# Performance work log

Measured on AMD Instinct MI355X. Metric: run time of the kernel, lower is better.

The kernel has to match this reference:

```python
import jax, jax.numpy as jnp
import numpy as np

DIM, HEADS, B, HT, WD = 96, 8, 4, 160, 160


def conv2d(x, w, b=None, padding=0, groups=1):
    out = jax.lax.conv_general_dilated(
        x, w, (1, 1), [(padding, padding), (padding, padding)],
        dimension_numbers=('NCHW', 'OIHW', 'NCHW'), feature_group_count=groups)
    if b is not None:
        out = out + b[None, :, None, None]
    return out


def setup_inputs() -> dict:
    key = jax.random.key(0)
    ks = jax.random.split(key, 16)
    dim, H = DIM, HEADS
    p = lambda i, shape: jax.random.normal(ks[i], shape, jnp.float32) * 0.05
    return {
        'x': jax.random.normal(ks[0], (B, dim, HT, WD), jnp.float32),
        'spectral': jax.random.normal(ks[1], (B, dim), jnp.float32),
        'temperature': jnp.ones((H, 1, 1), jnp.float32),
        'w_qkv': p(2, (3 * dim, dim, 1, 1)),           # 1x1x1 conv3d == 1x1 conv2d (depth=1)
        'w_dw': p(3, (3 * dim, 1, 3, 3)),              # middle depth slice of 3x3x3 dwconv
        'w_proj': p(4, (dim, dim, 1, 1)),
        'w_fc': p(5, (9, 3 * H)), 'b_fc': jnp.zeros((9,), jnp.float32),
        'w_dep': p(6, (dim, 9, 3, 3)), 'b_dep': jnp.zeros((dim,), jnp.float32),
        'w_se1': p(7, (2 * dim, dim)), 'b_se1': jnp.zeros((2 * dim,), jnp.float32),
        'w_se2': p(8, (dim, 2 * dim)), 'b_se2': jnp.zeros((dim,), jnp.float32),
        'w_saw1': p(9, (dim // 4, 1, 3, 3)), 'b_saw1': jnp.zeros((dim // 4,), jnp.float32),
        'w_saw2': p(10, (HEADS, dim // 4, 1, 1)), 'b_saw2': jnp.zeros((HEADS,), jnp.float32),
        'w_sgp': p(11, (dim, dim)), 'b_sgp': jnp.zeros((dim,), jnp.float32),
    }


def reference(x, spectral, temperature, w_qkv, w_dw, w_proj, w_fc, b_fc,
              w_dep, b_dep, w_se1, b_se1, w_se2, b_se2,
              w_saw1, b_saw1, w_saw2, b_saw2, w_sgp, b_sgp):
    b, c, h, w = x.shape
    H = temperature.shape[0]
    cH = c // H
    # spectral enhance gate: Linear -> GELU -> Linear -> Sigmoid
    sw = jax.nn.sigmoid(
        jax.nn.gelu(spectral @ w_se1.T + b_se1, approximate=False) @ w_se2.T + b_se2)
    x = x * sw[:, :, None, None]
    # qkv: 1x1 conv then 3x3 depthwise (depth-1 3D conv collapses to 2D middle slice)
    qkv = conv2d(conv2d(x, w_qkv), w_dw, padding=1, groups=3 * c)  # (b,3c,h,w)
    # fc branch: reshape (b,3c,h,w) -> (b,hw,3H,cH) -> (b,3H,hw,cH); 1x1 conv over 3H
    f_all = qkv.reshape(b, h * w, 3 * H, cH).transpose(0, 2, 1, 3)
    f_all = jnp.einsum('oc,bcnd->bond', w_fc, f_all) + b_fc[None, :, None, None]  # (b,9,hw,cH)
    f_conv = f_all.transpose(0, 3, 1, 2).reshape(b, 9 * cH, h, w)
    out_conv = conv2d(f_conv, w_dep, b_dep, padding=1, groups=cH)  # (b,c,h,w)
    # channel attention path
    q, k, v = jnp.split(qkv, 3, axis=1)
    resh = lambda t: t.reshape(b, H, cH, h * w)
    q, k, v = resh(q), resh(k), resh(v)
    sg = (spectral @ w_sgp.T + b_sgp).reshape(b, H, cH)
    cm = x.mean(axis=(1, 2, 3), keepdims=True)                      # (b,1,1,1)
    cm_exp = jnp.broadcast_to(cm, (b, 1, h, w))
    saw = jax.nn.sigmoid(conv2d(
        jax.nn.gelu(conv2d(cm_exp, w_saw1, b_saw1, padding=1), approximate=False),
        w_saw2, b_saw2))                                            # (b,H,h,w)
    saw = saw.mean(axis=(2, 3))[..., None]                          # (b,H,1)
    esg = sg * saw                                                  # (b,H,cH)
    sgm = esg[..., :, None] * esg[..., None, :]                     # (b,H,cH,cH)
    qn = q / jnp.maximum(jnp.linalg.norm(q, axis=-1, keepdims=True), 1e-12)
    kn = k / jnp.maximum(jnp.linalg.norm(k, axis=-1, keepdims=True), 1e-12)
    attn = jnp.einsum('bhcn,bhdn->bhcd', qn, kn) * temperature[None]
    attn = jax.nn.softmax(attn * sgm, axis=-1)
    out = jnp.einsum('bhcd,bhdn->bhcn', attn, v).reshape(b, c, h, w)
    out = conv2d(out, w_proj)
    return out + out_conv
```

## Files before the change

### kernel.cpp

```cpp
#include <hip/hip_runtime.h>
#include <math.h>

#define NB 4
#define C 96
#define C3 288
#define NH 8
#define CHD 12
#define HT 160
#define WD 160
#define HW 25600

typedef unsigned short u16;
typedef unsigned int   u32;
typedef __bf16 bf16x8 __attribute__((ext_vector_type(8)));
typedef float  f32x4  __attribute__((ext_vector_type(4)));

__device__ __forceinline__ float gelu_f(float x){
    return 0.5f * x * (1.0f + erff(x * 0.7071067811865475f));
}
__device__ __forceinline__ float sigmoid_f(float x){
    return 1.0f / (1.0f + expf(-x));
}
__device__ __forceinline__ u16 f2bf(float x){
    union { float f; u32 u; } v; v.f = x;
    u32 r = v.u + 0x7FFFu + ((v.u >> 16) & 1u);
    return (u16)(r >> 16);
}
__device__ __forceinline__ float bf2f(u16 s){
    union { u32 u; float f; } v; v.u = ((u32)s) << 16;
    return v.f;
}

__global__ __launch_bounds__(256) void k0_xsum(const float* __restrict__ x,
                                               float* __restrict__ xsum,
                                               u16* __restrict__ xb){
    int bc = blockIdx.x;
    const float4* p4 = (const float4*)(x + (size_t)bc * HW);
    u32* xo = (u32*)(xb + (size_t)bc * HW);
    float s = 0.f;
    for (int i = threadIdx.x; i < HW/4; i += 256){
        float4 v = p4[i];
        s += (v.x + v.y) + (v.z + v.w);
        xo[i*2]   = (u32)f2bf(v.x) | ((u32)f2bf(v.y) << 16);
        xo[i*2+1] = (u32)f2bf(v.z) | ((u32)f2bf(v.w) << 16);
    }
    __shared__ float red[256];
    red[threadIdx.x] = s;
    __syncthreads();
    for (int off = 128; off > 0; off >>= 1){
        if (threadIdx.x < off) red[threadIdx.x] += red[threadIdx.x + off];
        __syncthreads();
    }
    if (threadIdx.x == 0) xsum[bc] = red[0];
}

__global__ void k1_small(const float* __restrict__ spectral, const float* __restrict__ xsum,
                         const float* __restrict__ w_se1, const float* __restrict__ b_se1,
                         const float* __restrict__ w_se2, const float* __restrict__ b_se2,
                         const float* __restrict__ w_saw1, const float* __restrict__ b_saw1,
                         const float* __restrict__ w_saw2, const float* __restrict__ b_saw2,
                         const float* __restrict__ w_sgp, const float* __restrict__ b_sgp,
                         float* __restrict__ swg, float* __restrict__ esgg){
    __shared__ float spec[96];
    __shared__ float h1[192];
    __shared__ float cm_s;
    __shared__ float g1[9][24];
    __shared__ float saw[8];
    __shared__ float redbuf[96];
    int t = threadIdx.x;
    int b = blockIdx.x;
    if (t < 96) spec[t] = spectral[b*96 + t];
    __syncthreads();
    if (t < 192){
        float a = b_se1[t];
        for (int c = 0; c < 96; c++) a += spec[c] * w_se1[t*96 + c];
        h1[t] = gelu_f(a);
    }
    __syncthreads();
    if (t < 96){
        float a = b_se2[t];
        for (int j = 0; j < 192; j++) a += h1[j] * w_se2[t*192 + j];
        float s = sigmoid_f(a);
        swg[b*96 + t] = s;
        redbuf[t] = s * xsum[b*96 + t];
    }
    __syncthreads();
    if (t == 0){
        float cs = 0.f;
        for (int c = 0; c < 96; c++) cs += redbuf[c];
        cm_s = cs / (96.0f * (float)HW);
    }
    __syncthreads();
    float cm = cm_s;
    if (t < 9*24){
        int cat = t / 24, ch = t % 24;
        int ti = cat / 3, tj = cat % 3;
        float S = 0.f;
        for (int ki = 0; ki < 3; ki++){
            if (ti == 0 && ki == 0) continue;
            if (ti == 2 && ki == 2) continue;
            for (int kj = 0; kj < 3; kj++){
                if (tj == 0 && kj == 0) continue;
                if (tj == 2 && kj == 2) continue;
                S += w_saw1[ch*9 + ki*3 + kj];
            }
        }
        g1[cat][ch] = gelu_f(cm * S + b_saw1[ch]);
    }
    __syncthreads();
    if (t < 8){
        float acc = 0.f;
        const float cnt[3] = {1.f, 158.f, 1.f};
        for (int cat = 0; cat < 9; cat++){
            float a = b_saw2[t];
            for (int ch = 0; ch < 24; ch++) a += w_saw2[t*24 + ch] * g1[cat][ch];
            acc += cnt[cat/3] * cnt[cat%3] * sigmoid_f(a);
        }
        saw[t] = acc / (float)HW;
    }
    __syncthreads();
    if (t < 96){
        float a = b_sgp[t];
        for (int j = 0; j < 96; j++) a += spec[j] * w_sgp[t*96 + j];
        esgg[b*96 + t] = a * saw[t/12];
    }
}

__global__ __launch_bounds__(256) void k1w_weff(const float* __restrict__ w_qkv,
                                                const float* __restrict__ swg,
                                                u16* __restrict__ weffb){
    int b = blockIdx.x;
    int i = blockIdx.y * 256 + threadIdx.x;
    float w = w_qkv[i] * swg[b*96 + (i % 96)];
    weffb[(size_t)b*C3*96 + i] = f2bf(w);
}

__global__ __launch_bounds__(384) void k2a_mfma(const u16* __restrict__ xb,
                                                const u16* __restrict__ weffb,
                                                u16* __restrict__ Y,
                                                int bbase, long ystride){
    int b   = bbase + blockIdx.y;
    int px0 = blockIdx.x * 64;
    __shared__ u16 Xl[64*128];
    int t = threadIdx.x;
    const u32* xsrc = (const u32*)(xb + (size_t)b*C*HW + px0);
    for (int i = t; i < 96*32; i += 384){
        int c = i >> 5, pq = i & 31;
        u32 v = xsrc[(size_t)c*(HW/2) + pq];
        int slot = (((c >> 3) ^ (pq & 7)) << 3) + (c & 7);
        Xl[(2*pq)*128 + slot]     = (u16)(v & 0xffffu);
        Xl[(2*pq+1)*128 + slot]   = (u16)(v >> 16);
    }
    int wid = t >> 6, lane = t & 63;
    int lr = lane & 15, lk = lane >> 4;
    union U { uint4 q; bf16x8 v; };
    bf16x8 afr[3][3];
    const u16* wb = weffb + (size_t)b*C3*96;
    #pragma unroll
    for (int og = 0; og < 3; og++){
        int oc = og*96 + wid*16 + lr;
        #pragma unroll
        for (int kk = 0; kk < 3; kk++){
            U u; u.q = *(const uint4*)(wb + (size_t)oc*96 + kk*32 + lk*8);
            afr[og][kk] = u.v;
        }
    }
    __syncthreads();
    u16* Yb = Y + (size_t)blockIdx.y * ystride;
    #pragma unroll
    for (int sub = 0; sub < 4; sub++){
        int px = sub*16 + lr;
        int key = (px >> 1) & 7;
        bf16x8 bfr[3];
        #pragma unroll
        for (int kk = 0; kk < 3; kk++){
            int gs = (kk*4 + lk) ^ key;
            U u; u.q = *(const uint4*)(&Xl[px*128 + gs*8]);
            bfr[kk] = u.v;
        }
        #pragma unroll
        for (int og = 0; og < 3; og++){
            f32x4 acc = (f32x4){0.f,0.f,0.f,0.f};
            #pragma unroll
            for (int kk = 0; kk < 3; kk++)
                acc = __builtin_amdgcn_mfma_f32_16x16x32_bf16(afr[og][kk], bfr[kk], acc, 0, 0, 0);
            #pragma unroll
            for (int r = 0; r < 4; r++){
                int oc = og*96 + wid*16 + lk*4 + r;
                Yb[(size_t)oc*HW + px0 + sub*16 + lr] = f2bf(acc[r]);
            }
        }
    }
}

__global__ __launch_bounds__(256) void k2b_dw(const u16* __restrict__ Y,
                                              const float* __restrict__ w_dw,
                                              u16* __restrict__ qkv,
                                              int bbase, long ystride){
    int b  = bbase + blockIdx.z;
    int ch = blockIdx.y;
    int r0 = blockIdx.x * 8;
    __shared__ float tile[10*162];
    const u16* Yc = Y + (size_t)blockIdx.z*ystride + (size_t)ch*HW;
    int t = threadIdx.x;
    if (t < 10){ tile[t*162] = 0.f; tile[t*162 + 161] = 0.f; }
    for (int i = t; i < 800; i += 256){
        int r = i / 80, c2 = (i % 80) * 2;
        int gr = r0 + r - 1;
        u32 v = 0;
        if (gr >= 0 && gr < HT) v = *(const u32*)(Yc + gr*WD + c2);
        tile[r*162 + 1 + c2] = bf2f((u16)(v & 0xffffu));
        tile[r*162 + 2 + c2] = bf2f((u16)(v >> 16));
    }
    float w[9];
    #pragma unroll
    for (int k = 0; k < 9; k++) w[k] = w_dw[ch*9 + k];
    __syncthreads();
    u16* qc = qkv + ((size_t)b*C3 + ch)*HW + r0*WD;
    for (int i = t; i < 640; i += 256){
        int r = i / 80, c2 = (i % 80) * 2;
        float a0 = 0.f, a1 = 0.f;
        #pragma unroll
        for (int ki = 0; ki < 3; ki++){
            const float* row = &tile[(r+ki)*162 + c2];
            #pragma unroll
            for (int kj = 0; kj < 3; kj++){
                float wv = w[ki*3+kj];
                a0 += wv * row[kj];
                a1 += wv * row[kj+1];
            }
        }
        u32 pk = (u32)f2bf(a0) | ((u32)f2bf(a1) << 16);
        *(u32*)(qc + r*WD + c2) = pk;
    }
}

__global__ __launch_bounds__(256) void k3_mfma(const u16* __restrict__ qkv,
                                               const float* __restrict__ w_fc,
                                               const float* __restrict__ b_fc,
                                               u16* __restrict__ fws){
    int b  = blockIdx.y;
    int n0 = blockIdx.x * 64;
    __shared__ float wfc[216];
    __shared__ float bfc[9];
    __shared__ u16 ot[112*66];
    int t = threadIdx.x;
    if (t < 216) wfc[t] = w_fc[t];
    if (t < 9)   bfc[t] = b_fc[t];
    __syncthreads();
    int wv = t >> 6, lane = t & 63;
    int lr = lane & 15, lk = lane >> 4;
    int nrow = n0 + wv*16 + lr;
    const u16* rowp = qkv + (size_t)b*C3*HW + (size_t)nrow*288;
    union U { uint4 q; bf16x8 v; };
    U bfr[9];
    #pragma unroll
    for (int kk = 0; kk < 9; kk++)
        bfr[kk].q = *(const uint4*)(rowp + kk*32 + lk*8);

    for (int ct = 0; ct < 7; ct++){
        int coA = ct*16 + lr;
        int dA = coA / 9;
        int oA = coA - dA*9;
        f32x4 acc;
        #pragma unroll
        for (int r = 0; r < 4; r++){
            int coD = ct*16 + lk*4 + r;
            acc[r] = (coD < 108) ? bfc[coD % 9] : 0.f;
        }
        #pragma unroll
        for (int kk = 0; kk < 9; kk++){
            int base = kk*32 + lk*8;
            int bm = base % 12;
            int slot = dA - bm; slot += (slot < 0) ? 12 : 0;
            int j = base + slot;
            float wvl = (coA < 108 && slot < 8) ? wfc[oA*24 + j/12] : 0.f;
            u32 pk = ((u32)f2bf(wvl)) << ((slot & 1) * 16);
            int sh = slot >> 1;
            U a;
            a.q.x = (sh == 0) ? pk : 0u;
            a.q.y = (sh == 1) ? pk : 0u;
            a.q.z = (sh == 2) ? pk : 0u;
            a.q.w = (sh == 3) ? pk : 0u;
            acc = __builtin_amdgcn_mfma_f32_16x16x32_bf16(a.v, bfr[kk].v, acc, 0, 0, 0);
        }
        #pragma unroll
        for (int r = 0; r < 4; r++){
            int co = ct*16 + lk*4 + r;
            if (co < 108) ot[co*66 + wv*16 + lr] = f2bf(acc[r]);
        }
    }
    __syncthreads();
    const u32* otp = (const u32*)ot;
    u32* dst = (u32*)(fws + (size_t)b*108*HW + n0);
    for (int i = t; i < 108*32; i += 256){
        int pl = i >> 5, q = i & 31;
        dst[(size_t)pl*(HW/2) + q] = otp[pl*33 + q];
    }
}

__global__ __launch_bounds__(256) void k4_mfma(const u16* __restrict__ qkv,
                                               float* __restrict__ gpart){
    int b = blockIdx.z, h = blockIdx.y;
    int t = threadIdx.x;
    int wv = t >> 6, lane = t & 63;
    int lr = lane & 15, lk = lane >> 4;
    int row = (lr < 12) ? lr : 11;
    size_t pxb = (size_t)blockIdx.x*1024 + wv*256;
    const u16* qb = qkv + ((size_t)b*C3 + h*CHD + row)*HW + pxb;
    const u16* kb = qkv + ((size_t)b*C3 + C + h*CHD + row)*HW + pxb;
    union U { uint4 q; bf16x8 v; };
    f32x4 gqk = (f32x4){0.f,0.f,0.f,0.f};
    f32x4 gqq = (f32x4){0.f,0.f,0.f,0.f};
    f32x4 gkk = (f32x4){0.f,0.f,0.f,0.f};
    #pragma unroll
    for (int s = 0; s < 8; s++){
        U aq, ak;
        aq.q = *(const uint4*)(qb + s*32 + lk*8);
        ak.q = *(const uint4*)(kb + s*32 + lk*8);
        gqk = __builtin_amdgcn_mfma_f32_16x16x32_bf16(aq.v, ak.v, gqk, 0, 0, 0);
        gqq = __builtin_amdgcn_mfma_f32_16x16x32_bf16(aq.v, aq.v, gqq, 0, 0, 0);
        gkk = __builtin_amdgcn_mfma_f32_16x16x32_bf16(ak.v, ak.v, gkk, 0, 0, 0);
    }
    __shared__ float red[4][168];
    for (int i = t; i < 4*168; i += 256) ((float*)red)[i] = 0.f;
    __syncthreads();
    #pragma unroll
    for (int r = 0; r < 4; r++){
        int c = lk*4 + r;
        if (lr < 12 && c < 12){
            red[wv][c*12 + lr] = gqk[r];
            if (lr == c){
                red[wv][144 + c] = gqq[r];
                red[wv][156 + c] = gkk[r];
            }
        }
    }
    __syncthreads();
    if (t < 168){
        float a = red[0][t] + red[1][t] + red[2][t] + red[3][t];
        gpart[(((size_t)b*NH + h)*25 + blockIdx.x)*168 + t] = a;
    }
}

__global__ void k5_attn(const float* __restrict__ gpart, const float* __restrict__ esgg,
                        const float* __restrict__ temp, const float* __restrict__ w_proj,
                        u16* __restrict__ Mhib, u16* __restrict__ Mlob){
    int b = blockIdx.x;
    int t = threadIdx.x;
    __shared__ float G[NH][144];
    __shared__ float q2[NH][12], k2[NH][12];
    __shared__ float attn[NH][144];
    for (int i = t; i < NH*168; i += 256){
        int h = i / 168, e = i % 168;
        float a = 0.f;
        for (int ch = 0; ch < 25; ch++)
            a += gpart[(((size_t)b*NH + h)*25 + ch)*168 + e];
        if (e < 144)      G[h][e] = a;
        else if (e < 156) q2[h][e-144] = a;
        else              k2[h][e-156] = a;
    }
    __syncthreads();
    if (t < 96){
        int h = t / 12, c = t % 12;
        float rq  = 1.0f / fmaxf(sqrtf(q2[h][c]), 1e-12f);
        float tm  = temp[h];
        float egc = esgg[b*96 + h*12 + c];
        float lo[12];
        float mx = -1e30f;
        for (int d = 0; d < 12; d++){
            float rk = 1.0f / fmaxf(sqrtf(k2[h][d]), 1e-12f);
            float v = G[h][c*12 + d] * rq * rk * tm * (egc * esgg[b*96 + h*12 + d]);
            lo[d] = v;
            mx = fmaxf(mx, v);
        }
        float s = 0.f;
        for (int d = 0; d < 12; d++){ lo[d] = expf(lo[d] - mx); s += lo[d]; }
        float inv = 1.0f / s;
        for (int d = 0; d < 12; d++) attn[h][c*12 + d] = lo[d] * inv;
    }
    __syncthreads();
    for (int i = t; i < 96*96; i += 256){
        int co = i / 96, ci = i % 96;
        int h = ci / 12, d = ci % 12;
        float a = 0.f;
        #pragma unroll
        for (int c = 0; c < 12; c++)
            a += w_proj[co*96 + h*12 + c] * attn[h][c*12 + d];
        u16 hi = f2bf(a);
        float resid = a - bf2f(hi);
        Mhib[((size_t)b*96 + co)*96 + ci] = hi;
        Mlob[((size_t)b*96 + co)*96 + ci] = f2bf(resid);
    }
}

#define CP6 24
__global__ __launch_bounds__(256) void k6a_tap(const u16* __restrict__ fws,
                                               const float* __restrict__ w_dep,
                                               const float* __restrict__ b_dep,
                                               float* __restrict__ out){
    int b = blockIdx.z, d = blockIdx.y;
    int ty = blockIdx.x / 5, tx = blockIdx.x % 5;
    int r0 = ty*16, c0 = tx*32;
    __shared__ u16 inl[19*34*CP6];
    __shared__ u16 Wt2[16*160];
    int t = threadIdx.x;
    for (int i = t; i < (19*34*CP6)/2; i += 256) ((u32*)inl)[i] = 0u;
    __syncthreads();
    for (int i = t; i < 9*18*34; i += 256){
        int ch = i / 612, rem = i % 612, r = rem / 34, c = rem % 34;
        int gr = r0 + r - 1, gc = c0 + c - 1;
        u16 v = 0;
        if (gr >= 0 && gr < HT && gc >= 0 && gc < WD)
            v = fws[((size_t)(b*108 + d*9 + ch))*HW + gr*WD + gc];
        inl[(r*34 + c)*CP6 + ch] = v;
    }
    for (int i = t; i < 16*160; i += 256){
        int row = i / 160, k = i % 160;
        int tap = k >> 4, chp = k & 15;
        float wv = (row < 8 && tap < 9 && chp < 9)
                   ? w_dep[(size_t)(d*8 + row)*81 + chp*9 + tap] : 0.f;
        Wt2[i] = f2bf(wv);
    }
    __syncthreads();
    int wv = t >> 6, lane = t & 63;
    int lr = lane & 15, lk = lane >> 4;
    union U { uint4 q; bf16x8 v; };
    bf16x8 afr[5];
    #pragma unroll
    for (int kk = 0; kk < 5; kk++){
        U u; u.q = *(const uint4*)(&Wt2[lr*160 + kk*32 + lk*8]);
        afr[kk] = u.v;
    }
    int tap0 = lk >> 1;
    int h8   = (lk & 1) * 8;
    float binit[4];
    #pragma unroll
    for (int r = 0; r < 4; r++) binit[r] = (lk < 2) ? b_dep[d*8 + lk*4 + r] : 0.f;

    for (int gi = 0; gi < 8; gi++){
        int g = wv*8 + gi;
        int ry = g >> 1, half = g & 1;
        int cpx = half*16 + lr;
        f32x4 acc = (f32x4){binit[0], binit[1], binit[2], binit[3]};
        #pragma unroll
        for (int kk = 0; kk < 5; kk++){
            int tap = kk*2 + tap0;
            int ki = tap / 3, kj = tap - ki*3;
            U u; u.q = *(const uint4*)(&inl[((ry + ki)*34 + cpx + kj)*CP6 + h8]);
            acc = __builtin_amdgcn_mfma_f32_16x16x32_bf16(afr[kk], u.v, acc, 0, 0, 0);
        }
        if (lk < 2){
            #pragma unroll
            for (int r = 0; r < 4; r++){
                int oc = d*8 + lk*4 + r;
                out[((size_t)b*C + oc)*HW + (r0 + ry)*WD + c0 + cpx] = acc[r];
            }
        }
    }
}

__global__ __launch_bounds__(256) void k6b_mfma(const u16* __restrict__ qkv,
                                                const u16* __restrict__ Mhib,
                                                const u16* __restrict__ Mlob,
                                                float* __restrict__ out){
    int b   = blockIdx.y;
    int px0 = blockIdx.x * 64;
    __shared__ u16 Vl[64*128];
    int t = threadIdx.x;
    const u32* vsrc = (const u32*)(qkv + ((size_t)b*C3 + 2*C)*HW + px0);
    for (int i = t; i < 96*32; i += 256){
        int c = i >> 5, pq = i & 31;
        u32 v = vsrc[(size_t)c*(HW/2) + pq];
        int slot = (((c >> 3) ^ (pq & 7)) << 3) + (c & 7);
        Vl[(2*pq)*128 + slot]   = (u16)(v & 0xffffu);
        Vl[(2*pq+1)*128 + slot] = (u16)(v >> 16);
    }
    __syncthreads();
    int wid = t >> 6, lane = t & 63;
    int lr = lane & 15, lk = lane >> 4;
    union U { uint4 q; bf16x8 v; };
    int px = wid*16 + lr;
    int key = (px >> 1) & 7;
    bf16x8 bfr[3];
    #pragma unroll
    for (int kk = 0; kk < 3; kk++){
        int gs = (kk*4 + lk) ^ key;
        U u; u.q = *(const uint4*)(&Vl[px*128 + gs*8]);
        bfr[kk] = u.v;
    }
    const u16* mh = Mhib + (size_t)b*96*96;
    const u16* ml = Mlob + (size_t)b*96*96;
    for (int og = 0; og < 6; og++){
        int arow = og*16 + lr;
        f32x4 acc = (f32x4){0.f,0.f,0.f,0.f};
        #pragma unroll
        for (int kk = 0; kk < 3; kk++){
            U ah; ah.q = *(const uint4*)(mh + (size_t)arow*96 + kk*32 + lk*8);
            U al; al.q = *(const uint4*)(ml + (size_t)arow*96 + kk*32 + lk*8);
            acc = __builtin_amdgcn_mfma_f32_16x16x32_bf16(ah.v, bfr[kk], acc, 0, 0, 0);
            acc = __builtin_amdgcn_mfma_f32_16x16x32_bf16(al.v, bfr[kk], acc, 0, 0, 0);
        }
        #pragma unroll
        for (int r = 0; r < 4; r++){
            int oc = og*16 + lk*4 + r;
            float* op = out + ((size_t)b*C + oc)*HW + px0 + wid*16 + lr;
            *op += acc[r];
        }
    }
}

extern "C" void kernel_launch(void* const* d_in, const int* in_sizes, int n_in,
                              void* d_out, int out_size, void* d_ws, size_t ws_size,
                              hipStream_t stream){
    (void)in_sizes; (void)n_in; (void)out_size;
    const float* x           = (const float*)d_in[0];
    const float* spectral    = (const float*)d_in[1];
    const float* temperature = (const float*)d_in[2];
    const float* w_qkv       = (const float*)d_in[3];
    const float* w_dw        = (const float*)d_in[4];
    const float* w_proj      = (const float*)d_in[5];
    const float* w_fc        = (const float*)d_in[6];
    const float* b_fc        = (const float*)d_in[7];
    const float* w_dep       = (const float*)d_in[8];
    const float* b_dep       = (const float*)d_in[9];
    const float* w_se1       = (const float*)d_in[10];
    const float* b_se1       = (const float*)d_in[11];
    const float* w_se2       = (const float*)d_in[12];
    const float* b_se2       = (const float*)d_in[13];
    const float* w_saw1      = (const float*)d_in[14];
    const float* b_saw1      = (const float*)d_in[15];
    const float* w_saw2      = (const float*)d_in[16];
    const float* b_saw2      = (const float*)d_in[17];
    const float* w_sgp       = (const float*)d_in[18];
    const float* b_sgp       = (const float*)d_in[19];
    float* out = (float*)d_out;
    char* ws   = (char*)d_ws;

    const size_t QKV_B = 58982400ull;
    const size_t FWS_B = 22118400ull;
    const size_t XB_B  = 19660800ull;
    const size_t SM_B  = 1200000ull;
    const size_t Y_ONE = 14745600ull;
    bool fullY = ws_size >= QKV_B + 4*Y_ONE + FWS_B + XB_B + SM_B;
    size_t ybytes = fullY ? 4*Y_ONE : Y_ONE;

    u16*   qkv = (u16*)ws;
    u16*   Y   = (u16*)(ws + QKV_B);
    u16*   fws = (u16*)(ws + QKV_B + ybytes);
    u16*   xb  = (u16*)(ws + QKV_B + ybytes + FWS_B);
    float* sm  = (float*)(ws + QKV_B + ybytes + FWS_B + XB_B);
    float* xsum  = sm;
    float* swg   = sm + 384;
    float* esgg  = sm + 768;
    float* gpart = sm + 1152;
    u16*   weffb = (u16*)(sm + 135552);
    u16*   Mhib  = (u16*)((char*)weffb + 221184);
    u16*   Mlob  = (u16*)((char*)Mhib + 73728);

    k0_xsum <<<dim3(NB*C), dim3(256), 0, stream>>>(x, xsum, xb);
    k1_small<<<dim3(NB),   dim3(256), 0, stream>>>(spectral, xsum,
                w_se1, b_se1, w_se2, b_se2, w_saw1, b_saw1, w_saw2, b_saw2,
                w_sgp, b_sgp, swg, esgg);
    k1w_weff<<<dim3(NB,108), dim3(256), 0, stream>>>(w_qkv, swg, weffb);
    if (fullY){
        k2a_mfma<<<dim3(400,NB), dim3(384), 0, stream>>>(xb, weffb, Y, 0, (long)C3*HW);
        k2b_dw  <<<dim3(20,C3,NB), dim3(256), 0, stream>>>(Y, w_dw, qkv, 0, (long)C3*HW);
    } else {
        for (int b = 0; b < NB; b++){
            k2a_mfma<<<dim3(400,1), dim3(384), 0, stream>>>(xb, weffb, Y, b, 0);
            k2b_dw  <<<dim3(20,C3,1), dim3(256), 0, stream>>>(Y, w_dw, qkv, b, 0);
        }
    }
    k3_mfma <<<dim3(400,NB),   dim3(256), 0, stream>>>(qkv, w_fc, b_fc, fws);
    k4_mfma <<<dim3(25,NH,NB), dim3(256), 0, stream>>>(qkv, gpart);
    k5_attn <<<dim3(NB),       dim3(256), 0, stream>>>(gpart, esgg, temperature, w_proj, Mhib, Mlob);
    k6a_tap <<<dim3(50,12,NB), dim3(256), 0, stream>>>(fws, w_dep, b_dep, out);
    k6b_mfma<<<dim3(400,NB),   dim3(256), 0, stream>>>(qkv, Mhib, Mlob, out);
}
```

Measured before the change: 222.7 us.

## Store fc-branch output pixel-interleaved so depthwise tap kernel loads 16-byte vectors

The fc-branch kernel now writes its 108-channel result in a pixel-major layout padded to 16 channels per group (192 per pixel), with an XOR swizzle in shared memory. The tap kernel then loads each halo pixel's 9-channel group as two 16-byte vectors instead of nine scattered 2-byte gathers. The grid order is also changed so blocks that share the same spatial tile run next to each other, which is meant to improve cache reuse. Workspace buffers are rearranged so fws aliases Y or xb to fit the larger padded layout. The cost is extra bytes written for padding.

```diff
diff --git a/kernel.cpp b/kernel.cpp
--- a/kernel.cpp
+++ b/kernel.cpp
@@ -141,7 +141,7 @@
                                                 int bbase, long ystride){
     int b   = bbase + blockIdx.y;
     int px0 = blockIdx.x * 64;
-    __shared__ u16 Xl[64*128];
+    __shared__ __align__(16) u16 Xl[64*128];
     int t = threadIdx.x;
     const u32* xsrc = (const u32*)(xb + (size_t)b*C*HW + px0);
     for (int i = t; i < 96*32; i += 384){
@@ -243,15 +243,16 @@
     int n0 = blockIdx.x * 64;
     __shared__ float wfc[216];
     __shared__ float bfc[9];
-    __shared__ u16 ot[112*66];
+    __shared__ __align__(16) u16 ot[64*192];
     int t = threadIdx.x;
     if (t < 216) wfc[t] = w_fc[t];
     if (t < 9)   bfc[t] = b_fc[t];
+    for (int i = t; i < 64*96; i += 256) ((u32*)ot)[i] = 0u;
     __syncthreads();
     int wv = t >> 6, lane = t & 63;
     int lr = lane & 15, lk = lane >> 4;
-    int nrow = n0 + wv*16 + lr;
-    const u16* rowp = qkv + (size_t)b*C3*HW + (size_t)nrow*288;
+    int nl = wv*16 + lr;
+    const u16* rowp = qkv + (size_t)b*C3*HW + (size_t)(n0 + nl)*288;
     union U { uint4 q; bf16x8 v; };
     U bfr[9];
     #pragma unroll
@@ -287,15 +288,21 @@
         #pragma unroll
         for (int r = 0; r < 4; r++){
             int co = ct*16 + lk*4 + r;
-            if (co < 108) ot[co*66 + wv*16 + lr] = f2bf(acc[r]);
+            if (co < 108){
+                int dg = co / 9, o = co - dg*9;
+                int slot = dg*16 + o;
+                int p  = slot >> 1;
+                int ps = p ^ (nl & 7);
+                ot[nl*192 + (ps << 1) + (slot & 1)] = f2bf(acc[r]);
+            }
         }
     }
     __syncthreads();
     const u32* otp = (const u32*)ot;
-    u32* dst = (u32*)(fws + (size_t)b*108*HW + n0);
-    for (int i = t; i < 108*32; i += 256){
-        int pl = i >> 5, q = i & 31;
-        dst[(size_t)pl*(HW/2) + q] = otp[pl*33 + q];
+    u32* dst = (u32*)(fws + ((size_t)b*HW + n0)*192);
+    for (int i = t; i < 64*96; i += 256){
+        int nn = i / 96, s = i % 96;
+        dst[(size_t)nn*96 + s] = otp[nn*96 + (s ^ (nn & 7))];
     }
 }
 
@@ -395,25 +402,30 @@
 }
 
 #define CP6 24
-__global__ __launch_bounds__(256) void k6a_tap(const u16* __restrict__ fws,
-                                               const float* __restrict__ w_dep,
-                                               const float* __restrict__ b_dep,
-                                               float* __restrict__ out){
-    int b = blockIdx.z, d = blockIdx.y;
-    int ty = blockIdx.x / 5, tx = blockIdx.x % 5;
+__global__ __launch_bounds__(256) void k6a_iv(const u16* __restrict__ fws,
+                                              const float* __restrict__ w_dep,
+                                              const float* __restrict__ b_dep,
+                                              float* __restrict__ out){
+    int d = blockIdx.x, b = blockIdx.z;
+    int ty = blockIdx.y / 5, tx = blockIdx.y % 5;
     int r0 = ty*16, c0 = tx*32;
-    __shared__ u16 inl[19*34*CP6];
-    __shared__ u16 Wt2[16*160];
-    int t = threadIdx.x;
-    for (int i = t; i < (19*34*CP6)/2; i += 256) ((u32*)inl)[i] = 0u;
-    __syncthreads();
-    for (int i = t; i < 9*18*34; i += 256){
-        int ch = i / 612, rem = i % 612, r = rem / 34, c = rem % 34;
-        int gr = r0 + r - 1, gc = c0 + c - 1;
-        u16 v = 0;
-        if (gr >= 0 && gr < HT && gc >= 0 && gc < WD)
-            v = fws[((size_t)(b*108 + d*9 + ch))*HW + gr*WD + gc];
-        inl[(r*34 + c)*CP6 + ch] = v;
+    __shared__ __align__(16) u16 inl[19*34*CP6];
+    __shared__ __align__(16) u16 Wt2[16*160];
+    int t = threadIdx.x;
+    const uint4* fsrc = (const uint4*)fws;
+    for (int i = t; i < 646; i += 256){
+        uint4 v0 = make_uint4(0,0,0,0), v1 = make_uint4(0,0,0,0);
+        int p = i;
+        if (i < 612){
+            int r = i / 34, c = i - r*34;
+            int gr = r0 + r - 1, gc = c0 + c - 1;
+            if (gr >= 0 && gr < HT && gc >= 0 && gc < WD){
+                const uint4* src = fsrc + ((size_t)(b*HW + gr*WD + gc)*24 + d*2);
+                v0 = src[0]; v1 = src[1];
+            }
+        }
+        uint4* dstp = (uint4*)(&inl[p*CP6]);
+        dstp[0] = v0; dstp[1] = v1;
     }
     for (int i = t; i < 16*160; i += 256){
         int row = i / 160, k = i % 160;
@@ -466,7 +478,7 @@
                                                 float* __restrict__ out){
     int b   = blockIdx.y;
     int px0 = blockIdx.x * 64;
-    __shared__ u16 Vl[64*128];
+    __shared__ __align__(16) u16 Vl[64*128];
     int t = threadIdx.x;
     const u32* vsrc = (const u32*)(qkv + ((size_t)b*C3 + 2*C)*HW + px0);
     for (int i = t; i < 96*32; i += 256){
@@ -538,18 +550,26 @@
     char* ws   = (char*)d_ws;
 
     const size_t QKV_B = 58982400ull;
-    const size_t FWS_B = 22118400ull;
+    const size_t Y4    = 58982400ull;
+    const size_t Y1    = 14745600ull;
+    const size_t FWS_B = 39321600ull;
     const size_t XB_B  = 19660800ull;
-    const size_t SM_B  = 1200000ull;
-    const size_t Y_ONE = 14745600ull;
-    bool fullY = ws_size >= QKV_B + 4*Y_ONE + FWS_B + XB_B + SM_B;
-    size_t ybytes = fullY ? 4*Y_ONE : Y_ONE;
-
-    u16*   qkv = (u16*)ws;
-    u16*   Y   = (u16*)(ws + QKV_B);
-    u16*   fws = (u16*)(ws + QKV_B + ybytes);
-    u16*   xb  = (u16*)(ws + QKV_B + ybytes + FWS_B);
-    float* sm  = (float*)(ws + QKV_B + ybytes + FWS_B + XB_B);
+    const size_t SM_B  = 1000000ull;
+    bool fullY = ws_size >= QKV_B + Y4 + XB_B + SM_B;
+
+    u16 *qkv = (u16*)ws, *Y, *fws, *xb;
+    float* sm;
+    if (fullY){
+        Y   = (u16*)(ws + QKV_B);
+        fws = Y;
+        xb  = (u16*)(ws + QKV_B + Y4);
+        sm  = (float*)(ws + QKV_B + Y4 + XB_B);
+    } else {
+        Y   = (u16*)(ws + QKV_B);
+        xb  = (u16*)(ws + QKV_B + Y1);
+        fws = xb;
+        sm  = (float*)(ws + QKV_B + Y1 + FWS_B);
+    }
     float* xsum  = sm;
     float* swg   = sm + 384;
     float* esgg  = sm + 768;
@@ -575,6 +595,6 @@
     k3_mfma <<<dim3(400,NB),   dim3(256), 0, stream>>>(qkv, w_fc, b_fc, fws);
     k4_mfma <<<dim3(25,NH,NB), dim3(256), 0, stream>>>(qkv, gpart);
     k5_attn <<<dim3(NB),       dim3(256), 0, stream>>>(gpart, esgg, temperature, w_proj, Mhib, Mlob);
-    k6a_tap <<<dim3(50,12,NB), dim3(256), 0, stream>>>(fws, w_dep, b_dep, out);
+    k6a_iv  <<<dim3(12,50,NB), dim3(256), 0, stream>>>(fws, w_dep, b_dep, out);
     k6b_mfma<<<dim3(400,NB),   dim3(256), 0, stream>>>(qkv, Mhib, Mlob, out);
 }
```

New measurement: 225.8 us. Within noise of the previous version (+1.4%).
